# Kernel tuning notes

Measured on AMD Instinct MI355X. Metric: run time of the kernel, lower is better.

The kernel has to match this reference:

```python
import jax, jax.numpy as jnp
import numpy as np
from jax import lax

B, L, D, E, K, H = 8, 1024, 256, 8, 2, 1024  # batch, seq(in_channel), in_dim, experts, top_k, out_channel/hidden
LMAX = L // 2  # largest expert input dim (factor i+2 = 2)
LENS = [L // (i + 2) for i in range(E)]


def setup_inputs() -> dict:
    key = jax.random.key(0)
    ks = jax.random.split(key, 12)
    x = jax.random.normal(ks[0], (B, L, D), dtype=jnp.float32)
    conv_ws = jax.random.normal(ks[1], (3, D, D, 3), dtype=jnp.float32) / np.sqrt(3 * D)
    conv_bs = jax.random.normal(ks[2], (3, D), dtype=jnp.float32) * 0.01
    fl_w = jax.random.normal(ks[3], (E, L), dtype=jnp.float32) / np.sqrt(L)
    fl_b = jax.random.normal(ks[4], (E,), dtype=jnp.float32) * 0.01
    # expert first-layer weights, zero-padded on input axis to LMAX (expert i uses L//(i+2) inputs)
    w1 = jax.random.normal(ks[5], (E, H, LMAX), dtype=jnp.float32) / np.sqrt(LMAX)
    col_mask = (np.arange(LMAX)[None, :] < np.array(LENS)[:, None]).astype(np.float32)  # [E, LMAX]
    w1 = w1 * jnp.asarray(col_mask)[:, None, :]
    b1 = jax.random.normal(ks[6], (E, H), dtype=jnp.float32) * 0.01
    w2 = jax.random.normal(ks[7], (E, H, H), dtype=jnp.float32) / np.sqrt(H)
    b2 = jax.random.normal(ks[8], (E, H), dtype=jnp.float32) * 0.01
    w3 = jax.random.normal(ks[9], (E, H, H), dtype=jnp.float32) / np.sqrt(H)
    b3 = jax.random.normal(ks[10], (E, H), dtype=jnp.float32) * 0.01
    return {"x": x, "conv_ws": conv_ws, "conv_bs": conv_bs, "fl_w": fl_w, "fl_b": fl_b,
            "w1": w1, "b1": b1, "w2": w2, "b2": b2, "w3": w3, "b3": b3}


def _gelu(v):
    return jax.nn.gelu(v, approximate=False)  # torch nn.GELU default is exact erf


def _forward(x, conv_ws, conv_bs, fl_w, fl_b, w1, b1, w2, b2, w3, b3):
    xt = jnp.transpose(x, (0, 2, 1))  # [B, D, L]
    # --- Router: 3 dilated causal-padded ('same') convs + GELU ---
    h = xt
    for i in range(3):
        d = 2 ** i
        h = lax.conv_general_dilated(h, conv_ws[i], window_strides=(1,), padding=[(d, d)],
                                     rhs_dilation=(d,), dimension_numbers=("NCH", "OIH", "NCH"))
        h = _gelu(h + conv_bs[i][None, :, None])
    logits = jax.nn.sigmoid(jnp.einsum("bdl,el->bde", h, fl_w) + fl_b)  # [B, D, E]
    prob = jax.nn.softmax(logits, axis=-1)
    top_val, top_idx = lax.top_k(prob, K)  # [B, D, K]
    top_val = top_val / jnp.sum(top_val, axis=-1, keepdims=True)
    # combine gate per expert: gates[b,d,e] = sum_k top_val * 1[top_idx==e]
    gates = jnp.sum(top_val[..., None] * jax.nn.one_hot(top_idx, E, dtype=top_val.dtype), axis=2)  # [B, D, E]
    # --- Per-expert downsample (avg_pool1d, kernel=stride=i+2), zero-padded to LMAX ---
    xs = []
    for i in range(E):
        f = i + 2
        Li = LENS[i]
        xd = xt[:, :, :Li * f].reshape(B, D, Li, f).mean(-1)  # [B, D, Li]
        xs.append(jnp.pad(xd, ((0, 0), (0, 0), (0, LMAX - Li))))
    xe = jnp.stack(xs)  # [E, B, D, LMAX]; pad cols align with zeroed w1 cols
    # --- Expert MLPs (dense compute, masked by gates; zero gate == token not routed) ---
    h1 = _gelu(jnp.einsum("ebdl,ehl->ebdh", xe, w1) + b1[:, None, None, :])
    h2 = _gelu(jnp.einsum("ebdh,egh->ebdg", h1, w2) + b2[:, None, None, :])
    h3 = jnp.einsum("ebdg,eog->ebdo", h2, w3) + b3[:, None, None, :]  # [E, B, D, H]
    out = jnp.einsum("ebdo,bde->bdo", h3, gates)  # scatter-add combine, [B, D, H]
    return jnp.transpose(out, (0, 2, 1))  # [B, L(out_channel), D]


def reference(x, conv_ws, conv_bs, fl_w, fl_b, w1, b1, w2, b2, w3, b3):
    return _forward(x, conv_ws, conv_bs, fl_w, fl_b, w1, b1, w2, b2, w3, b3)
```

## Files before the change

### kernel.cpp

```cpp
#include <hip/hip_runtime.h>
#include <math.h>

#define Bb 8
#define Ll 1024
#define Dd 256
#define Ee 8
#define Hh 1024
#define LMAXc 512
#define NTOK (Bb*Dd)
#define LPAD 1032
#define MAXTILES 72

typedef short bf16x8 __attribute__((ext_vector_type(8)));
typedef float f32x4 __attribute__((ext_vector_type(4)));
typedef unsigned short u16x8 __attribute__((ext_vector_type(8)));

__device__ __forceinline__ float gelu_f(float x) {
    return 0.5f * x * (1.0f + erff(x * 0.70710678118654752440f));
}
__device__ __forceinline__ unsigned short f2b(float x) {
    unsigned int u = __float_as_uint(x);
    return (unsigned short)((u + 0x7fffu + ((u >> 16) & 1u)) >> 16);
}
__device__ __forceinline__ float b2f(unsigned short h) {
    return __uint_as_float(((unsigned int)h) << 16);
}
__device__ __forceinline__ void gl_lds16(const void* g, void* l) {
    __builtin_amdgcn_global_load_lds((const __attribute__((address_space(1))) unsigned int*)g,
                                     (__attribute__((address_space(3))) unsigned int*)l, 16, 0, 0);
}
__device__ __forceinline__ void split_one4(const float* __restrict__ src,
                                           unsigned short* __restrict__ hi,
                                           unsigned short* __restrict__ lo, int idx) {
    float4 v = ((const float4*)src)[idx];
    ushort2 h01, h23, l01, l23;
    unsigned short h;
    h = f2b(v.x); h01.x = h; l01.x = f2b(v.x - b2f(h));
    h = f2b(v.y); h01.y = h; l01.y = f2b(v.y - b2f(h));
    h = f2b(v.z); h23.x = h; l23.x = f2b(v.z - b2f(h));
    h = f2b(v.w); h23.y = h; l23.y = f2b(v.w - b2f(h));
    ((ushort2*)hi)[idx * 2] = h01; ((ushort2*)hi)[idx * 2 + 1] = h23;
    ((ushort2*)lo)[idx * 2] = l01; ((ushort2*)lo)[idx * 2 + 1] = l23;
}
__device__ __forceinline__ void cvt_one4(const float* __restrict__ src,
                                         unsigned short* __restrict__ dst, int idx) {
    float4 v = ((const float4*)src)[idx];
    ushort2 h01, h23;
    h01.x = f2b(v.x); h01.y = f2b(v.y);
    h23.x = f2b(v.z); h23.y = f2b(v.w);
    ((ushort2*)dst)[idx * 2] = h01; ((ushort2*)dst)[idx * 2 + 1] = h23;
}

__global__ __launch_bounds__(256) void prep_all(
    const float* __restrict__ x, const float* __restrict__ cw,
    const float* __restrict__ w1, const float* __restrict__ w2,
    const float* __restrict__ w3,
    unsigned short* __restrict__ xhi, unsigned short* __restrict__ xlo,
    unsigned short* __restrict__ chi, unsigned short* __restrict__ clo,
    unsigned short* __restrict__ wchi, unsigned short* __restrict__ wclo,
    unsigned short* __restrict__ w1hi, unsigned short* __restrict__ w1lo,
    unsigned short* __restrict__ w2b, unsigned short* __restrict__ w3b,
    unsigned short* __restrict__ xe)
{
    int blk = blockIdx.x;
    int t = threadIdx.x;
    if (blk < 2048) {
        int idx = blk * 256 + t;
        int d4 = idx & 63;
        int l  = (idx >> 6) & 1023;
        int b  = idx >> 16;
        float4 v = ((const float4*)x)[idx];
        size_t o = ((size_t)(b * LPAD + 4 + l) * Dd + d4 * 4) >> 1;
        ushort2 h01, h23, l01, l23;
        unsigned short h;
        h = f2b(v.x); h01.x = h; l01.x = f2b(v.x - b2f(h));
        h = f2b(v.y); h01.y = h; l01.y = f2b(v.y - b2f(h));
        h = f2b(v.z); h23.x = h; l23.x = f2b(v.z - b2f(h));
        h = f2b(v.w); h23.y = h; l23.y = f2b(v.w - b2f(h));
        ((ushort2*)xhi)[o] = h01; ((ushort2*)xhi)[o + 1] = h23;
        ((ushort2*)xlo)[o] = l01; ((ushort2*)xlo)[o + 1] = l23;
    } else if (blk < 4352) {
        int idx = (blk - 2048) * 256 + t;
        int i = idx & (Dd - 1);
        int o = (idx >> 8) & (Dd - 1);
        int lk = idx >> 16;
        int layer = lk / 3;
        int k = lk % 3;
        float v = cw[(((size_t)layer * Dd + o) * Dd + i) * 3 + k];
        unsigned short h = f2b(v);
        wchi[idx] = h;
        wclo[idx] = f2b(v - b2f(h));
    } else if (blk < 8448) {
        split_one4(w1, w1hi, w1lo, (blk - 4352) * 256 + t);
    } else if (blk < 16640) {
        cvt_one4(w2, w2b, (blk - 8448) * 256 + t);
    } else if (blk < 24832) {
        cvt_one4(w3, w3b, (blk - 16640) * 256 + t);
    } else if (blk < 24864) {
        int u = (blk - 24832) * 256 + t;
        int f = u >> 11;
        int rem = u & 2047;
        int b = rem >> 8;
        int r2 = rem & 255;
        int row = r2 >> 5;
        int col = (r2 & 31) * 8;
        int padrow = (row < 4) ? row : (1024 + row);
        unsigned short* buf = (f == 0) ? xhi : (f == 1) ? xlo : (f == 2) ? chi : clo;
        u16x8 z = {0, 0, 0, 0, 0, 0, 0, 0};
        *(u16x8*)(buf + (size_t)(b * LPAD + padrow) * Dd + col) = z;
    } else {
        int u = blk - 24864;
        int e = u >> 9;
        int b = (u >> 6) & 7;
        int c = u & 63;
        int f = e + 2;
        int Li = Ll / f;
        int j0 = c * 8;
        if (j0 >= Li) return;
        int d = t;
        float invf = 1.0f / (float)f;
        int lim = Li - 1;
        float v[8] = {};
        for (int r = 0; r < f; ++r) {
            #pragma unroll
            for (int jj = 0; jj < 8; ++jj) {
                int j = j0 + jj; if (j > lim) j = lim;
                v[jj] += x[((size_t)(b * Ll + j * f + r)) * Dd + d];
            }
        }
        size_t obase = ((size_t)(e * NTOK + b * 256 + d)) * LMAXc + j0;
        if (j0 + 8 <= Li) {
            u16x8 hv;
            #pragma unroll
            for (int q = 0; q < 8; ++q) hv[q] = (short)f2b(v[q] * invf);
            *(u16x8*)(xe + obase) = hv;
        } else {
            for (int jj = 0; jj < Li - j0; ++jj)
                xe[obase + jj] = f2b(v[jj] * invf);
        }
    }
}

template<int MODE>
__global__ __launch_bounds__(256, 2) void conv_mfma(
    const unsigned short* __restrict__ inhi, const unsigned short* __restrict__ inlo,
    const unsigned short* __restrict__ whiL, const unsigned short* __restrict__ wloL,
    const float* __restrict__ bias,
    unsigned short* __restrict__ outhi, unsigned short* __restrict__ outlo,
    float* __restrict__ outf, int dil)
{
    __shared__ char smem[32768];
    char* sAhi = smem;
    char* sAlo = smem + 8192;
    char* sBhi = smem + 16384;
    char* sBlo = smem + 24576;

    const int t = threadIdx.x;
    const int lane = t & 63, w = t >> 6;
    const int r16 = lane & 15, quad = lane >> 4;
    const int wr = w >> 1, wc = w & 1;
    const int row0 = blockIdx.x * 64;
    const int col0 = blockIdx.y * 64;
    const int b = row0 >> 10, l0 = row0 & 1023;

    int aoff[2], boff[2];
    #pragma unroll
    for (int i = 0; i < 2; ++i) {
        int ra = wr * 32 + i * 16 + r16;
        aoff[i] = ra * 64 + ((quad ^ ((ra >> 1) & 3)) << 4);
        int rb = wc * 32 + i * 16 + r16;
        boff[i] = rb * 64 + ((quad ^ ((rb >> 1) & 3)) << 4);
    }
    const int rs = t >> 2, ce = ((t & 3) ^ ((rs >> 1) & 3)) << 3;
    const unsigned short* gAhi = inhi + (size_t)(b * LPAD + 4 + l0 + rs) * Dd + ce;
    const unsigned short* gAlo = inlo + (size_t)(b * LPAD + 4 + l0 + rs) * Dd + ce;

    f32x4 acc[2][2];
    const f32x4 zero4 = {0.f, 0.f, 0.f, 0.f};
    #pragma unroll
    for (int i = 0; i < 2; ++i)
        #pragma unroll
        for (int j = 0; j < 2; ++j) acc[i][j] = zero4;

    for (int tap = 0; tap < 3; ++tap) {
        const int sh = (tap - 1) * dil;
        const unsigned short* pAhi = gAhi + sh * Dd;
        const unsigned short* pAlo = gAlo + sh * Dd;
        const unsigned short* gBhi = whiL + ((size_t)tap * Dd + col0 + rs) * Dd + ce;
        const unsigned short* gBlo = wloL + ((size_t)tap * Dd + col0 + rs) * Dd + ce;
        for (int kb = 0; kb < Dd; kb += 64) {
            gl_lds16(pAhi + kb,      sAhi + (w << 10));
            gl_lds16(pAhi + kb + 32, sAhi + 4096 + (w << 10));
            gl_lds16(pAlo + kb,      sAlo + (w << 10));
            gl_lds16(pAlo + kb + 32, sAlo + 4096 + (w << 10));
            gl_lds16(gBhi + kb,      sBhi + (w << 10));
            gl_lds16(gBhi + kb + 32, sBhi + 4096 + (w << 10));
            gl_lds16(gBlo + kb,      sBlo + (w << 10));
            gl_lds16(gBlo + kb + 32, sBlo + 4096 + (w << 10));
            __syncthreads();
            #pragma unroll
            for (int h = 0; h < 2; ++h) {
                const int ho = h * 4096;
                bf16x8 ah[2], al[2], bh[2], bl[2];
                #pragma unroll
                for (int i = 0; i < 2; ++i) {
                    ah[i] = *(const bf16x8*)(sAhi + ho + aoff[i]);
                    al[i] = *(const bf16x8*)(sAlo + ho + aoff[i]);
                    bh[i] = *(const bf16x8*)(sBhi + ho + boff[i]);
                    bl[i] = *(const bf16x8*)(sBlo + ho + boff[i]);
                }
                #pragma unroll
                for (int mi = 0; mi < 2; ++mi)
                    #pragma unroll
                    for (int ni = 0; ni < 2; ++ni) {
                        acc[mi][ni] = __builtin_amdgcn_mfma_f32_16x16x32_bf16(ah[mi], bh[ni], acc[mi][ni], 0, 0, 0);
                        acc[mi][ni] = __builtin_amdgcn_mfma_f32_16x16x32_bf16(ah[mi], bl[ni], acc[mi][ni], 0, 0, 0);
                        acc[mi][ni] = __builtin_amdgcn_mfma_f32_16x16x32_bf16(al[mi], bh[ni], acc[mi][ni], 0, 0, 0);
                    }
            }
            __syncthreads();
        }
    }

    int cc[2]; float bv[2];
    #pragma unroll
    for (int ni = 0; ni < 2; ++ni) {
        cc[ni] = col0 + wc * 32 + ni * 16 + r16;
        bv[ni] = bias[cc[ni]];
    }
    #pragma unroll
    for (int mi = 0; mi < 2; ++mi) {
        int lb = l0 + wr * 32 + mi * 16 + quad * 4;
        #pragma unroll
        for (int reg = 0; reg < 4; ++reg) {
            int l = lb + reg;
            #pragma unroll
            for (int ni = 0; ni < 2; ++ni) {
                float v = gelu_f(acc[mi][ni][reg] + bv[ni]);
                if (MODE == 0) {
                    size_t o = (size_t)(b * LPAD + 4 + l) * Dd + cc[ni];
                    unsigned short h = f2b(v);
                    outhi[o] = h;
                    outlo[o] = f2b(v - b2f(h));
                } else {
                    outf[(size_t)(b * Ll + l) * Dd + cc[ni]] = v;
                }
            }
        }
    }
}

template<int MODE, int GATHER, int TWOPASS>
__global__ __launch_bounds__(256, 4) void gemm_sp(
    const unsigned short* __restrict__ AG,
    const unsigned short* __restrict__ BhiG, const unsigned short* __restrict__ BloG,
    const float* __restrict__ biasG, const float* __restrict__ gates,
    const int* __restrict__ cntG, const int* __restrict__ listG,
    const int* __restrict__ tileTab, const int* __restrict__ ntiles,
    unsigned short* __restrict__ Cout, float* __restrict__ outf,
    int M, int N, int K)
{
    if (blockIdx.y >= ntiles[0]) return;
    const int desc = tileTab[blockIdx.y];
    const int e = desc >> 16;
    const int row0 = (desc & 0xffff) * 64;
    const int cn = cntG[e];

    constexpr int NCH = TWOPASS ? 2 : 4;
    __shared__ char smem[TWOPASS ? 24576 : 32768];
    char* sA   = smem;
    char* sBhi = smem + NCH * 4096;
    char* sBlo = smem + 2 * NCH * 4096;

    const unsigned short* Bhi = BhiG + (size_t)e * N * K;
    const unsigned short* Blo = TWOPASS ? (BloG + (size_t)e * N * K) : nullptr;
    const float* bias = biasG + (size_t)e * N;

    int Keff = K;
    if (GATHER) {
        int Li = Ll / (e + 2);
        Keff = ((Li + 63) >> 6) << 6;
    }

    const int t = threadIdx.x;
    const int lane = t & 63, w = t >> 6;
    const int r16 = lane & 15, quad = lane >> 4;
    const int wr = w >> 1, wc = w & 1;
    const int col0 = blockIdx.x * 64;

    int aoff[2], boff[2];
    #pragma unroll
    for (int i = 0; i < 2; ++i) {
        int ra = wr * 32 + i * 16 + r16;
        aoff[i] = ra * 64 + ((quad ^ ((ra >> 1) & 3)) << 4);
        int rb = wc * 32 + i * 16 + r16;
        boff[i] = rb * 64 + ((quad ^ ((rb >> 1) & 3)) << 4);
    }
    const int r0s = t >> 2, c0s = ((t & 3) ^ ((r0s >> 1) & 3)) << 3;
    int ri = row0 + r0s; if (ri > cn - 1) ri = cn - 1;
    const int ar = GATHER ? listG[e * NTOK + ri] : ri;
    const unsigned short* gA  = AG + ((size_t)e * M + ar) * K + c0s;
    const unsigned short* gB  = Bhi + (size_t)(col0 + r0s) * K + c0s;
    const unsigned short* gBl = TWOPASS ? (Blo + (size_t)(col0 + r0s) * K + c0s) : nullptr;
    const int wofs = w << 10;

    f32x4 acc[2][2];
    const f32x4 zero4 = {0.f, 0.f, 0.f, 0.f};
    #pragma unroll
    for (int i = 0; i < 2; ++i)
        #pragma unroll
        for (int j = 0; j < 2; ++j) acc[i][j] = zero4;

    for (int k0 = 0; k0 < Keff; k0 += NCH * 32) {
        #pragma unroll
        for (int c = 0; c < NCH; ++c) {
            gl_lds16(gA + k0 + c * 32, sA + c * 4096 + wofs);
            gl_lds16(gB + k0 + c * 32, sBhi + c * 4096 + wofs);
        }
        if (TWOPASS) {
            #pragma unroll
            for (int c = 0; c < NCH; ++c)
                gl_lds16(gBl + k0 + c * 32, sBlo + c * 4096 + wofs);
        }
        __syncthreads();
        #pragma unroll
        for (int h = 0; h < NCH; ++h) {
            const int ho = h * 4096;
            bf16x8 ah[2], bh[2];
            #pragma unroll
            for (int i = 0; i < 2; ++i) {
                ah[i] = *(const bf16x8*)(sA + ho + aoff[i]);
                bh[i] = *(const bf16x8*)(sBhi + ho + boff[i]);
            }
            #pragma unroll
            for (int mi = 0; mi < 2; ++mi)
                #pragma unroll
                for (int ni = 0; ni < 2; ++ni)
                    acc[mi][ni] = __builtin_amdgcn_mfma_f32_16x16x32_bf16(ah[mi], bh[ni], acc[mi][ni], 0, 0, 0);
            if (TWOPASS) {
                bf16x8 bl[2];
                #pragma unroll
                for (int i = 0; i < 2; ++i) bl[i] = *(const bf16x8*)(sBlo + ho + boff[i]);
                #pragma unroll
                for (int mi = 0; mi < 2; ++mi)
                    #pragma unroll
                    for (int ni = 0; ni < 2; ++ni)
                        acc[mi][ni] = __builtin_amdgcn_mfma_f32_16x16x32_bf16(ah[mi], bl[ni], acc[mi][ni], 0, 0, 0);
            }
        }
        __syncthreads();
    }

    int cc[2]; float bv[2];
    #pragma unroll
    for (int ni = 0; ni < 2; ++ni) {
        cc[ni] = col0 + wc * 32 + ni * 16 + r16;
        bv[ni] = bias[cc[ni]];
    }
    if (MODE == 0) {
        unsigned short* CE = Cout + (size_t)e * M * N;
        #pragma unroll
        for (int mi = 0; mi < 2; ++mi) {
            int rb = row0 + wr * 32 + mi * 16 + quad * 4;
            #pragma unroll
            for (int reg = 0; reg < 4; ++reg) {
                size_t roff = (size_t)(rb + reg) * N;
                #pragma unroll
                for (int ni = 0; ni < 2; ++ni)
                    CE[roff + cc[ni]] = f2b(gelu_f(acc[mi][ni][reg] + bv[ni]));
            }
        }
    } else {
        #pragma unroll
        for (int mi = 0; mi < 2; ++mi) {
            int rb = row0 + wr * 32 + mi * 16 + quad * 4;
            #pragma unroll
            for (int reg = 0; reg < 4; ++reg) {
                int i = rb + reg;
                if (i < cn) {
                    int tok = listG[e * NTOK + i];
                    float g = gates[(size_t)tok * Ee + e];
                    size_t roff = (size_t)tok * N;
                    #pragma unroll
                    for (int ni = 0; ni < 2; ++ni)
                        atomicAdd(&outf[roff + cc[ni]], g * (acc[mi][ni][reg] + bv[ni]));
                }
            }
        }
    }
}


__global__ __launch_bounds__(256) void logits_accum(const float* __restrict__ h,
                                                    const float* __restrict__ fl_w,
                                                    float* __restrict__ logits) {
    int b = blockIdx.x;
    int chunk = blockIdx.y;
    __shared__ float wsm[Ee][128];
    for (int i = threadIdx.x; i < Ee * 128; i += 256) {
        int e = i >> 7, l = i & 127;
        wsm[e][l] = fl_w[e * Ll + chunk * 128 + l];
    }
    __syncthreads();
    int d = threadIdx.x;
    float acc[Ee] = {};
    for (int l = 0; l < 128; ++l) {
        float v = h[((size_t)b * Ll + chunk * 128 + l) * Dd + d];
        #pragma unroll
        for (int e = 0; e < Ee; ++e) acc[e] += v * wsm[e][l];
    }
    int tok = b * Dd + d;
    #pragma unroll
    for (int e = 0; e < Ee; ++e) atomicAdd(&logits[tok * Ee + e], acc[e]);
}

__global__ __launch_bounds__(1024) void gates_final(const float* __restrict__ logits,
                                                    const float* __restrict__ fl_b,
                                                    float* __restrict__ gates,
                                                    int* __restrict__ cnt,
                                                    int* __restrict__ list,
                                                    int* __restrict__ tileTab,
                                                    int* __restrict__ ntiles) {
    __shared__ int scnt[Ee];
    if (threadIdx.x < Ee) scnt[threadIdx.x] = 0;
    __syncthreads();
    const int lane = threadIdx.x & 63;
    const unsigned long long ltmask = (1ull << lane) - 1ull;

    for (int tok = threadIdx.x; tok < NTOK; tok += 1024) {
        float s[Ee];
        #pragma unroll
        for (int e = 0; e < Ee; ++e) {
            float z = logits[tok * Ee + e] + fl_b[e];
            s[e] = 1.0f / (1.0f + expf(-z));
        }
        float mx = s[0];
        #pragma unroll
        for (int e = 1; e < Ee; ++e) mx = fmaxf(mx, s[e]);
        float p[Ee];
        #pragma unroll
        for (int e = 0; e < Ee; ++e) p[e] = expf(s[e] - mx);
        int i1 = 0;
        #pragma unroll
        for (int e = 1; e < Ee; ++e) if (p[e] > p[i1]) i1 = e;
        int i2 = (i1 == 0) ? 1 : 0;
        #pragma unroll
        for (int e = 0; e < Ee; ++e) {
            if (e == i1 || e == i2) continue;
            if (p[e] > p[i2]) i2 = e;
        }
        float inv = 1.0f / (p[i1] + p[i2]);
        #pragma unroll
        for (int e = 0; e < Ee; ++e) gates[tok * Ee + e] = 0.0f;
        gates[tok * Ee + i1] = p[i1] * inv;
        gates[tok * Ee + i2] = p[i2] * inv;

        #pragma unroll
        for (int slot = 0; slot < 2; ++slot) {
            int ie = slot ? i2 : i1;
            for (int e = 0; e < Ee; ++e) {
                unsigned long long m = __ballot(ie == e);
                if (m) {
                    int leader = __ffsll((long long)m) - 1;
                    int base = 0;
                    if (lane == leader) base = atomicAdd(&scnt[e], (int)__popcll(m));
                    base = __shfl(base, leader);
                    if (ie == e) {
                        int pos = base + (int)__popcll(m & ltmask);
                        list[e * NTOK + pos] = tok;
                    }
                }
            }
        }
    }
    __syncthreads();
    if (threadIdx.x < Ee) cnt[threadIdx.x] = scnt[threadIdx.x];
    if (threadIdx.x == 0) {
        int nt = 0;
        for (int e = 0; e < Ee; ++e) {
            int c = scnt[e];
            for (int m = 0; m * 64 < c; ++m) tileTab[nt++] = (e << 16) | m;
        }
        ntiles[0] = nt;
    }
}

__global__ __launch_bounds__(256) void transpose_out(const float* __restrict__ outacc,
                                                     float* __restrict__ out) {
    __shared__ float tile[32][33];
    int b = blockIdx.z;
    int d0 = blockIdx.x * 32;
    int o0 = blockIdx.y * 32;
    int tx = threadIdx.x & 31, ty = threadIdx.x >> 5;
    for (int i = 0; i < 32; i += 8)
        tile[ty + i][tx] = outacc[((size_t)b * Dd + d0 + ty + i) * Hh + o0 + tx];
    __syncthreads();
    for (int i = 0; i < 32; i += 8)
        out[((size_t)b * Hh + o0 + ty + i) * Dd + d0 + tx] = tile[tx][ty + i];
}

extern "C" void kernel_launch(void* const* d_in, const int* in_sizes, int n_in,
                              void* d_out, int out_size, void* d_ws, size_t ws_size,
                              hipStream_t stream) {
    const float* x       = (const float*)d_in[0];
    const float* conv_w  = (const float*)d_in[1];
    const float* conv_b  = (const float*)d_in[2];
    const float* fl_w    = (const float*)d_in[3];
    const float* fl_b    = (const float*)d_in[4];
    const float* w1      = (const float*)d_in[5];
    const float* b1      = (const float*)d_in[6];
    const float* w2      = (const float*)d_in[7];
    const float* b2      = (const float*)d_in[8];
    const float* w3      = (const float*)d_in[9];
    const float* b3      = (const float*)d_in[10];
    float* out = (float*)d_out;

    char* ws = (char*)d_ws;
    unsigned short* xphi = (unsigned short*)(ws);
    unsigned short* xplo = (unsigned short*)(ws + 4227072);
    unsigned short* cphi = (unsigned short*)(ws + 8454144);
    unsigned short* cplo = (unsigned short*)(ws + 12681216);
    unsigned short* wchi = (unsigned short*)(ws + 16908288);
    unsigned short* wclo = (unsigned short*)(ws + 18087936);
    float* hL            = (float*)(ws + 19267584);
    unsigned short* h1   = (unsigned short*)(ws);
    unsigned short* h2   = (unsigned short*)(ws + 33554432);
    unsigned short* xe   = (unsigned short*)(ws + 67108864);
    unsigned short* w1hi = (unsigned short*)(ws + 83886080);
    unsigned short* w1lo = (unsigned short*)(ws + 92274688);
    unsigned short* w2b  = (unsigned short*)(ws + 100663296);
    unsigned short* w3b  = (unsigned short*)(ws + 117440512);
    float* logits  = (float*)(ws + 134217728);
    int*   cnt     = (int*)(ws + 134283264);
    int*   ntiles  = (int*)(ws + 134283296);
    int*   tileTab = (int*)(ws + 134283328);
    float* gates   = (float*)(ws + 134284288);
    int*   list    = (int*)(ws + 134349824);
    float* outacc  = (float*)(ws);

    hipMemsetAsync(logits, 0, 65536 + 64, stream);

    prep_all<<<28960, 256, 0, stream>>>(x, conv_w, w1, w2, w3,
                                        xphi, xplo, cphi, cplo, wchi, wclo,
                                        w1hi, w1lo, w2b, w3b, xe);

    const int WL = 3 * Dd * Dd;
    conv_mfma<0><<<dim3(Bb * Ll / 64, Dd / 64), 256, 0, stream>>>(
        xphi, xplo, wchi + 0 * WL, wclo + 0 * WL, conv_b + 0 * Dd, cphi, cplo, nullptr, 1);
    conv_mfma<0><<<dim3(Bb * Ll / 64, Dd / 64), 256, 0, stream>>>(
        cphi, cplo, wchi + 1 * WL, wclo + 1 * WL, conv_b + 1 * Dd, xphi, xplo, nullptr, 2);
    conv_mfma<1><<<dim3(Bb * Ll / 64, Dd / 64), 256, 0, stream>>>(
        xphi, xplo, wchi + 2 * WL, wclo + 2 * WL, conv_b + 2 * Dd, nullptr, nullptr, hL, 4);

    logits_accum<<<dim3(Bb, 8), 256, 0, stream>>>(hL, fl_w, logits);
    gates_final<<<1, 1024, 0, stream>>>(logits, fl_b, gates, cnt, list, tileTab, ntiles);

    gemm_sp<0, 1, 1><<<dim3(16, MAXTILES), 256, 0, stream>>>(
        xe, w1hi, w1lo, b1, nullptr, cnt, list, tileTab, ntiles, h1, nullptr, NTOK, Hh, LMAXc);

    gemm_sp<0, 0, 0><<<dim3(16, MAXTILES), 256, 0, stream>>>(
        h1, w2b, nullptr, b2, nullptr, cnt, list, tileTab, ntiles, h2, nullptr, NTOK, Hh, Hh);

    hipMemsetAsync(outacc, 0, (size_t)NTOK * Hh * sizeof(float), stream);

    gemm_sp<1, 0, 0><<<dim3(16, MAXTILES), 256, 0, stream>>>(
        h2, w3b, nullptr, b3, gates, cnt, list, tileTab, ntiles, nullptr, outacc, NTOK, Hh, Hh);

    transpose_out<<<dim3(Dd / 32, Hh / 32, Bb), 256, 0, stream>>>(outacc, out);
}
```

Baseline: 313.9 us.

## Fuse router logits projection into last conv epilogue and batch prep loads

The third conv layer no longer writes its fp32 GELU output to global memory. Its epilogue multiplies the tile by the fl_w slice held in LDS, reduces partial logits with shared-memory atomics, and atomically adds them into the global logits, which removes the separate logits_accum kernel and its 8 MB round trip. The prep kernel is also reordered: the downsample blocks come first, and each thread in the conversion blocks now handles four float4 loads to raise memory-level parallelism, so the grid shrinks. In exchange the conv epilogue gains LDS atomics and more global atomics, and the floating-point summation order changes.

```diff
diff --git a/kernel.cpp b/kernel.cpp
--- a/kernel.cpp
+++ b/kernel.cpp
@@ -29,10 +29,9 @@
     __builtin_amdgcn_global_load_lds((const __attribute__((address_space(1))) unsigned int*)g,
                                      (__attribute__((address_space(3))) unsigned int*)l, 16, 0, 0);
 }
-__device__ __forceinline__ void split_one4(const float* __restrict__ src,
-                                           unsigned short* __restrict__ hi,
-                                           unsigned short* __restrict__ lo, int idx) {
-    float4 v = ((const float4*)src)[idx];
+__device__ __forceinline__ void split_store(float4 v,
+                                            unsigned short* __restrict__ hi,
+                                            unsigned short* __restrict__ lo, int idx) {
     ushort2 h01, h23, l01, l23;
     unsigned short h;
     h = f2b(v.x); h01.x = h; l01.x = f2b(v.x - b2f(h));
@@ -42,9 +41,7 @@
     ((ushort2*)hi)[idx * 2] = h01; ((ushort2*)hi)[idx * 2 + 1] = h23;
     ((ushort2*)lo)[idx * 2] = l01; ((ushort2*)lo)[idx * 2 + 1] = l23;
 }
-__device__ __forceinline__ void cvt_one4(const float* __restrict__ src,
-                                         unsigned short* __restrict__ dst, int idx) {
-    float4 v = ((const float4*)src)[idx];
+__device__ __forceinline__ void cvt_store(float4 v, unsigned short* __restrict__ dst, int idx) {
     ushort2 h01, h23;
     h01.x = f2b(v.x); h01.y = f2b(v.y);
     h23.x = f2b(v.z); h23.y = f2b(v.w);
@@ -64,52 +61,8 @@
 {
     int blk = blockIdx.x;
     int t = threadIdx.x;
-    if (blk < 2048) {
-        int idx = blk * 256 + t;
-        int d4 = idx & 63;
-        int l  = (idx >> 6) & 1023;
-        int b  = idx >> 16;
-        float4 v = ((const float4*)x)[idx];
-        size_t o = ((size_t)(b * LPAD + 4 + l) * Dd + d4 * 4) >> 1;
-        ushort2 h01, h23, l01, l23;
-        unsigned short h;
-        h = f2b(v.x); h01.x = h; l01.x = f2b(v.x - b2f(h));
-        h = f2b(v.y); h01.y = h; l01.y = f2b(v.y - b2f(h));
-        h = f2b(v.z); h23.x = h; l23.x = f2b(v.z - b2f(h));
-        h = f2b(v.w); h23.y = h; l23.y = f2b(v.w - b2f(h));
-        ((ushort2*)xhi)[o] = h01; ((ushort2*)xhi)[o + 1] = h23;
-        ((ushort2*)xlo)[o] = l01; ((ushort2*)xlo)[o + 1] = l23;
-    } else if (blk < 4352) {
-        int idx = (blk - 2048) * 256 + t;
-        int i = idx & (Dd - 1);
-        int o = (idx >> 8) & (Dd - 1);
-        int lk = idx >> 16;
-        int layer = lk / 3;
-        int k = lk % 3;
-        float v = cw[(((size_t)layer * Dd + o) * Dd + i) * 3 + k];
-        unsigned short h = f2b(v);
-        wchi[idx] = h;
-        wclo[idx] = f2b(v - b2f(h));
-    } else if (blk < 8448) {
-        split_one4(w1, w1hi, w1lo, (blk - 4352) * 256 + t);
-    } else if (blk < 16640) {
-        cvt_one4(w2, w2b, (blk - 8448) * 256 + t);
-    } else if (blk < 24832) {
-        cvt_one4(w3, w3b, (blk - 16640) * 256 + t);
-    } else if (blk < 24864) {
-        int u = (blk - 24832) * 256 + t;
-        int f = u >> 11;
-        int rem = u & 2047;
-        int b = rem >> 8;
-        int r2 = rem & 255;
-        int row = r2 >> 5;
-        int col = (r2 & 31) * 8;
-        int padrow = (row < 4) ? row : (1024 + row);
-        unsigned short* buf = (f == 0) ? xhi : (f == 1) ? xlo : (f == 2) ? chi : clo;
-        u16x8 z = {0, 0, 0, 0, 0, 0, 0, 0};
-        *(u16x8*)(buf + (size_t)(b * LPAD + padrow) * Dd + col) = z;
-    } else {
-        int u = blk - 24864;
+    if (blk < 4096) {
+        int u = blk;
         int e = u >> 9;
         int b = (u >> 6) & 7;
         int c = u & 63;
@@ -138,6 +91,80 @@
             for (int jj = 0; jj < Li - j0; ++jj)
                 xe[obase + jj] = f2b(v[jj] * invf);
         }
+    } else if (blk < 4128) {
+        int u = (blk - 4096) * 256 + t;
+        int f = u >> 11;
+        int rem = u & 2047;
+        int b = rem >> 8;
+        int r2 = rem & 255;
+        int row = r2 >> 5;
+        int col = (r2 & 31) * 8;
+        int padrow = (row < 4) ? row : (1024 + row);
+        unsigned short* buf = (f == 0) ? xhi : (f == 1) ? xlo : (f == 2) ? chi : clo;
+        u16x8 z = {0, 0, 0, 0, 0, 0, 0, 0};
+        *(u16x8*)(buf + (size_t)(b * LPAD + padrow) * Dd + col) = z;
+    } else if (blk < 4640) {
+        int base = (blk - 4128) * 1024 + t;
+        float4 v[4];
+        #pragma unroll
+        for (int it = 0; it < 4; ++it) v[it] = ((const float4*)x)[base + it * 256];
+        #pragma unroll
+        for (int it = 0; it < 4; ++it) {
+            int idx = base + it * 256;
+            int d4 = idx & 63;
+            int l  = (idx >> 6) & 1023;
+            int b  = idx >> 16;
+            size_t o = ((size_t)(b * LPAD + 4 + l) * Dd + d4 * 4) >> 1;
+            ushort2 h01, h23, l01, l23;
+            unsigned short h;
+            h = f2b(v[it].x); h01.x = h; l01.x = f2b(v[it].x - b2f(h));
+            h = f2b(v[it].y); h01.y = h; l01.y = f2b(v[it].y - b2f(h));
+            h = f2b(v[it].z); h23.x = h; l23.x = f2b(v[it].z - b2f(h));
+            h = f2b(v[it].w); h23.y = h; l23.y = f2b(v[it].w - b2f(h));
+            ((ushort2*)xhi)[o] = h01; ((ushort2*)xhi)[o + 1] = h23;
+            ((ushort2*)xlo)[o] = l01; ((ushort2*)xlo)[o + 1] = l23;
+        }
+    } else if (blk < 5216) {
+        int base = (blk - 4640) * 1024 + t;
+        float vv[4];
+        #pragma unroll
+        for (int it = 0; it < 4; ++it) {
+            int idx = base + it * 256;
+            int i = idx & (Dd - 1);
+            int o = (idx >> 8) & (Dd - 1);
+            int lk = idx >> 16;
+            int layer = lk / 3;
+            int k = lk % 3;
+            vv[it] = cw[(((size_t)layer * Dd + o) * Dd + i) * 3 + k];
+        }
+        #pragma unroll
+        for (int it = 0; it < 4; ++it) {
+            int idx = base + it * 256;
+            unsigned short h = f2b(vv[it]);
+            wchi[idx] = h;
+            wclo[idx] = f2b(vv[it] - b2f(h));
+        }
+    } else if (blk < 6240) {
+        int base = (blk - 5216) * 1024 + t;
+        float4 v[4];
+        #pragma unroll
+        for (int it = 0; it < 4; ++it) v[it] = ((const float4*)w1)[base + it * 256];
+        #pragma unroll
+        for (int it = 0; it < 4; ++it) split_store(v[it], w1hi, w1lo, base + it * 256);
+    } else if (blk < 8288) {
+        int base = (blk - 6240) * 1024 + t;
+        float4 v[4];
+        #pragma unroll
+        for (int it = 0; it < 4; ++it) v[it] = ((const float4*)w2)[base + it * 256];
+        #pragma unroll
+        for (int it = 0; it < 4; ++it) cvt_store(v[it], w2b, base + it * 256);
+    } else {
+        int base = (blk - 8288) * 1024 + t;
+        float4 v[4];
+        #pragma unroll
+        for (int it = 0; it < 4; ++it) v[it] = ((const float4*)w3)[base + it * 256];
+        #pragma unroll
+        for (int it = 0; it < 4; ++it) cvt_store(v[it], w3b, base + it * 256);
     }
 }
 
@@ -147,7 +174,7 @@
     const unsigned short* __restrict__ whiL, const unsigned short* __restrict__ wloL,
     const float* __restrict__ bias,
     unsigned short* __restrict__ outhi, unsigned short* __restrict__ outlo,
-    float* __restrict__ outf, int dil)
+    const float* __restrict__ flw, float* __restrict__ logits, int dil)
 {
     __shared__ char smem[32768];
     char* sAhi = smem;
@@ -228,24 +255,60 @@
         cc[ni] = col0 + wc * 32 + ni * 16 + r16;
         bv[ni] = bias[cc[ni]];
     }
-    #pragma unroll
-    for (int mi = 0; mi < 2; ++mi) {
-        int lb = l0 + wr * 32 + mi * 16 + quad * 4;
-        #pragma unroll
-        for (int reg = 0; reg < 4; ++reg) {
-            int l = lb + reg;
-            #pragma unroll
-            for (int ni = 0; ni < 2; ++ni) {
-                float v = gelu_f(acc[mi][ni][reg] + bv[ni]);
-                if (MODE == 0) {
+    if (MODE == 0) {
+        #pragma unroll
+        for (int mi = 0; mi < 2; ++mi) {
+            int lb = l0 + wr * 32 + mi * 16 + quad * 4;
+            #pragma unroll
+            for (int reg = 0; reg < 4; ++reg) {
+                int l = lb + reg;
+                #pragma unroll
+                for (int ni = 0; ni < 2; ++ni) {
+                    float v = gelu_f(acc[mi][ni][reg] + bv[ni]);
                     size_t o = (size_t)(b * LPAD + 4 + l) * Dd + cc[ni];
                     unsigned short h = f2b(v);
                     outhi[o] = h;
                     outlo[o] = f2b(v - b2f(h));
-                } else {
-                    outf[(size_t)(b * Ll + l) * Dd + cc[ni]] = v;
                 }
             }
+        }
+    } else {
+        float* wl   = (float*)smem;
+        float* slog = (float*)(smem + 2048);
+        for (int i = t; i < 512; i += 256) {
+            int ll = i >> 3, e = i & 7;
+            wl[i] = flw[e * Ll + l0 + ll];
+            slog[i] = 0.0f;
+        }
+        __syncthreads();
+        float part[2][8];
+        #pragma unroll
+        for (int ni = 0; ni < 2; ++ni)
+            #pragma unroll
+            for (int e = 0; e < 8; ++e) part[ni][e] = 0.0f;
+        #pragma unroll
+        for (int mi = 0; mi < 2; ++mi) {
+            #pragma unroll
+            for (int reg = 0; reg < 4; ++reg) {
+                int ll = wr * 32 + mi * 16 + quad * 4 + reg;
+                #pragma unroll
+                for (int ni = 0; ni < 2; ++ni) {
+                    float v = gelu_f(acc[mi][ni][reg] + bv[ni]);
+                    #pragma unroll
+                    for (int e = 0; e < 8; ++e) part[ni][e] += v * wl[ll * 8 + e];
+                }
+            }
+        }
+        #pragma unroll
+        for (int ni = 0; ni < 2; ++ni) {
+            int dl = wc * 32 + ni * 16 + r16;
+            #pragma unroll
+            for (int e = 0; e < 8; ++e) atomicAdd(&slog[dl * 8 + e], part[ni][e]);
+        }
+        __syncthreads();
+        for (int i = t; i < 512; i += 256) {
+            int dl = i >> 3, e = i & 7;
+            atomicAdd(&logits[(size_t)(b * Dd + col0 + dl) * Ee + e], slog[i]);
         }
     }
 }
@@ -391,29 +454,6 @@
 }
 
 
-__global__ __launch_bounds__(256) void logits_accum(const float* __restrict__ h,
-                                                    const float* __restrict__ fl_w,
-                                                    float* __restrict__ logits) {
-    int b = blockIdx.x;
-    int chunk = blockIdx.y;
-    __shared__ float wsm[Ee][128];
-    for (int i = threadIdx.x; i < Ee * 128; i += 256) {
-        int e = i >> 7, l = i & 127;
-        wsm[e][l] = fl_w[e * Ll + chunk * 128 + l];
-    }
-    __syncthreads();
-    int d = threadIdx.x;
-    float acc[Ee] = {};
-    for (int l = 0; l < 128; ++l) {
-        float v = h[((size_t)b * Ll + chunk * 128 + l) * Dd + d];
-        #pragma unroll
-        for (int e = 0; e < Ee; ++e) acc[e] += v * wsm[e][l];
-    }
-    int tok = b * Dd + d;
-    #pragma unroll
-    for (int e = 0; e < Ee; ++e) atomicAdd(&logits[tok * Ee + e], acc[e]);
-}
-
 __global__ __launch_bounds__(1024) void gates_final(const float* __restrict__ logits,
                                                     const float* __restrict__ fl_b,
                                                     float* __restrict__ gates,
@@ -522,7 +562,6 @@
     unsigned short* cplo = (unsigned short*)(ws + 12681216);
     unsigned short* wchi = (unsigned short*)(ws + 16908288);
     unsigned short* wclo = (unsigned short*)(ws + 18087936);
-    float* hL            = (float*)(ws + 19267584);
     unsigned short* h1   = (unsigned short*)(ws);
     unsigned short* h2   = (unsigned short*)(ws + 33554432);
     unsigned short* xe   = (unsigned short*)(ws + 67108864);
@@ -540,19 +579,18 @@
 
     hipMemsetAsync(logits, 0, 65536 + 64, stream);
 
-    prep_all<<<28960, 256, 0, stream>>>(x, conv_w, w1, w2, w3,
+    prep_all<<<10336, 256, 0, stream>>>(x, conv_w, w1, w2, w3,
                                         xphi, xplo, cphi, cplo, wchi, wclo,
                                         w1hi, w1lo, w2b, w3b, xe);
 
     const int WL = 3 * Dd * Dd;
     conv_mfma<0><<<dim3(Bb * Ll / 64, Dd / 64), 256, 0, stream>>>(
-        xphi, xplo, wchi + 0 * WL, wclo + 0 * WL, conv_b + 0 * Dd, cphi, cplo, nullptr, 1);
+        xphi, xplo, wchi + 0 * WL, wclo + 0 * WL, conv_b + 0 * Dd, cphi, cplo, nullptr, nullptr, 1);
     conv_mfma<0><<<dim3(Bb * Ll / 64, Dd / 64), 256, 0, stream>>>(
-        cphi, cplo, wchi + 1 * WL, wclo + 1 * WL, conv_b + 1 * Dd, xphi, xplo, nullptr, 2);
+        cphi, cplo, wchi + 1 * WL, wclo + 1 * WL, conv_b + 1 * Dd, xphi, xplo, nullptr, nullptr, 2);
     conv_mfma<1><<<dim3(Bb * Ll / 64, Dd / 64), 256, 0, stream>>>(
-        xphi, xplo, wchi + 2 * WL, wclo + 2 * WL, conv_b + 2 * Dd, nullptr, nullptr, hL, 4);
-
-    logits_accum<<<dim3(Bb, 8), 256, 0, stream>>>(hL, fl_w, logits);
+        xphi, xplo, wchi + 2 * WL, wclo + 2 * WL, conv_b + 2 * Dd, nullptr, nullptr, fl_w, logits, 4);
+
     gates_final<<<1, 1024, 0, stream>>>(logits, fl_b, gates, cnt, list, tileTab, ntiles);
 
     gemm_sp<0, 1, 1><<<dim3(16, MAXTILES), 256, 0, stream>>>(
```

New measurement: 308.2 us. No clear change (-1.8%).
